# Kernel optimization log

Measured on AMD Instinct MI355X. Metric: run time of the kernel, lower is better.

The kernel has to match this reference:

```python
import jax, jax.numpy as jnp
import numpy as np

C = 64
NUM_HEADS = 8
HEAD_DIM = C // NUM_HEADS


def setup_inputs() -> dict:
    key = jax.random.key(0)
    ks = jax.random.split(key, 8)
    B, D, H, W = 1, 8, 24, 32
    s = 1.0 / np.sqrt(C)  # conv3d default init scale (approx)
    return {
        "x": jax.random.normal(ks[0], (B, C, D, H, W), dtype=jnp.float32),
        "wq": jax.random.normal(ks[1], (C, C), dtype=jnp.float32) * s,
        "bq": jax.random.normal(ks[2], (C,), dtype=jnp.float32) * s,
        "wk": jax.random.normal(ks[3], (C, C), dtype=jnp.float32) * s,
        "bk": jax.random.normal(ks[4], (C,), dtype=jnp.float32) * s,
        "wv": jax.random.normal(ks[5], (C, C), dtype=jnp.float32) * s,
        "bv": jax.random.normal(ks[6], (C,), dtype=jnp.float32) * s,
        "gamma": jnp.zeros((1,), dtype=jnp.float32),
    }


def _proj(x_flat, w, b):
    # x_flat: [B, C, N]; 1x1x1 conv == channel-mixing matmul
    return jnp.einsum("oc,bcn->bon", w, x_flat) + b[None, :, None]


def reference(x, wq, bq, wk, bk, wv, bv, gamma):
    B, Cc, D, Hh, W = x.shape
    N = D * Hh * W
    xf = x.reshape(B, Cc, N)
    # [B, heads, head_dim, N]
    q = _proj(xf, wq, bq).reshape(B, NUM_HEADS, HEAD_DIM, N)
    k = _proj(xf, wk, bk).reshape(B, NUM_HEADS, HEAD_DIM, N)
    v = _proj(xf, wv, bv).reshape(B, NUM_HEADS, HEAD_DIM, N)
    scale = 1.0 / np.sqrt(HEAD_DIM)
    # energy: [B, heads, N, N] = q^T k
    energy = jnp.einsum("bhdn,bhdm->bhnm", q, k) * scale
    attn = jax.nn.softmax(energy, axis=-1)
    # out: [B, heads, head_dim, N]
    out = jnp.einsum("bhnm,bhdm->bhdn", attn, v)
    out = out.reshape(B, Cc, D, Hh, W)
    return gamma * out + x
```

## Files before the change

### kernel.cpp

```cpp
#include <hip/hip_runtime.h>
#include <hip/hip_bf16.h>

typedef __attribute__((ext_vector_type(8)))  short  short8;
typedef __attribute__((ext_vector_type(16))) float  f32x16;

#define N_TOK 6144
#define NHEADS 8
#define TK 256
#define VPITCH (TK + 8)
#define QTILES 24

static __device__ __forceinline__ ushort f2bf(float f) {
    union { __hip_bfloat16 h; ushort u; } c;
    c.h = __float2bfloat16(f);
    return c.u;
}

static __device__ __forceinline__ uint packexp2(float s0, float s1) {
    float t0 = __builtin_fmaf(s0, 128.0f, 12599161.0f);
    float t1 = __builtin_fmaf(s1, 128.0f, 12599161.0f);
    return __builtin_amdgcn_perm(__float_as_uint(t1), __float_as_uint(t0), 0x05040100u);
}

__global__ __launch_bounds__(256)
void proj_kernel(const float* __restrict__ x,
                 const float* __restrict__ wq, const float* __restrict__ bq,
                 const float* __restrict__ wk, const float* __restrict__ bk,
                 const float* __restrict__ wv, const float* __restrict__ bv,
                 ushort* __restrict__ Qb, ushort* __restrict__ Kb, ushort* __restrict__ Vt)
{
    __shared__ float wql[512], wkl[512], wvl[512];
    const int b  = blockIdx.x;
    const int h  = b / 24;
    const int nt = b % 24;
    const int t  = threadIdx.x;

    for (int i = t; i < 512; i += 256) {
        int row = i >> 6, col = i & 63;
        wql[i] = wq[(h * 8 + row) * 64 + col];
        wkl[i] = wk[(h * 8 + row) * 64 + col];
        wvl[i] = wv[(h * 8 + row) * 64 + col];
    }
    __syncthreads();

    const int n = nt * 256 + t;
    float accq[8], acck[8], accv[8];
#pragma unroll
    for (int d = 0; d < 8; ++d) { accq[d] = 0.f; acck[d] = 0.f; accv[d] = 0.f; }

    for (int c = 0; c < 64; c += 4) {
        float x0 = x[(c + 0) * N_TOK + n];
        float x1 = x[(c + 1) * N_TOK + n];
        float x2 = x[(c + 2) * N_TOK + n];
        float x3 = x[(c + 3) * N_TOK + n];
#pragma unroll
        for (int d = 0; d < 8; ++d) {
            float4 wqv = *(const float4*)&wql[d * 64 + c];
            float4 wkv = *(const float4*)&wkl[d * 64 + c];
            float4 wvv = *(const float4*)&wvl[d * 64 + c];
            accq[d] += wqv.x * x0 + wqv.y * x1 + wqv.z * x2 + wqv.w * x3;
            acck[d] += wkv.x * x0 + wkv.y * x1 + wkv.z * x2 + wkv.w * x3;
            accv[d] += wvv.x * x0 + wvv.y * x1 + wvv.z * x2 + wvv.w * x3;
        }
    }

    const float qscale = 0.5100700982081662f;
    union { ushort us[8]; uint4 v; } qo, ko;
#pragma unroll
    for (int d = 0; d < 8; ++d) {
        qo.us[d] = f2bf((accq[d] + bq[h * 8 + d]) * qscale);
        ko.us[d] = f2bf(acck[d] + bk[h * 8 + d]);
    }
    size_t base = ((size_t)h * N_TOK + n) * 8;
    *(uint4*)&Qb[base] = qo.v;
    *(uint4*)&Kb[base] = ko.v;

    const int j  = n & 15;
    const int jp = ((j & 12) == 4) ? j + 4 : (((j & 12) == 8) ? j - 4 : j);
    const int np = (n & ~15) | jp;
#pragma unroll
    for (int d = 0; d < 8; ++d)
        Vt[((size_t)(h * 8 + d)) * N_TOK + np] = f2bf(accv[d] + bv[h * 8 + d]);
}

__global__ __launch_bounds__(256)
void attn_kernel(const ushort* __restrict__ Qb, const ushort* __restrict__ Kb,
                 const ushort* __restrict__ Vt,
                 float* __restrict__ partL, float* __restrict__ partO,
                 int KS, int NK)
{
    __shared__ __align__(16) ushort Klds[TK * 8];
    __shared__ __align__(16) ushort Vlds[9 * VPITCH];

    const int b     = blockIdx.x;
    const int slice = b / (NHEADS * QTILES);
    const int rem   = b - slice * (NHEADS * QTILES);
    const int h     = rem / QTILES;
    const int qt    = rem - h * QTILES;
    const int tid   = threadIdx.x;
    const int lane  = tid & 63;
    const int qi    = lane & 31;
    const int hi    = lane >> 5;
    const int q0    = qt * 256 + (tid >> 6) * 64 + qi;

    {
        uint* v8 = (uint*)&Vlds[8 * VPITCH];
        if (tid < 128) v8[tid] = 0x3F803F80u;
    }

    union { uint4 u; short8 s; } qf0, qf1;
    qf0.u = make_uint4(0u, 0u, 0u, 0u);
    qf1.u = make_uint4(0u, 0u, 0u, 0u);
    if (hi == 0) {
        qf0.u = *(const uint4*)&Qb[((size_t)h * N_TOK + q0) * 8];
        qf1.u = *(const uint4*)&Qb[((size_t)h * N_TOK + q0 + 32) * 8];
    }

    f32x16 o0, o1, zc;
#pragma unroll
    for (int i = 0; i < 16; ++i) { o0[i] = 0.f; o1[i] = 0.f; zc[i] = 0.f; }

    const ushort* kbase = &Klds[qi * 8];
    const int     vrow  = (qi < 8) ? qi : 8;
    const ushort* vbase = &Vlds[vrow * VPITCH + hi * 8];
    const int     k0g   = slice * NK;

    const uint4* kg = (const uint4*)&Kb[((size_t)h * N_TOK + k0g) * 8];
    const uint4* vg = (const uint4*)&Vt[((size_t)(h * 8 + (tid >> 5))) * N_TOK + k0g];
    const int    vchunk = tid & 31;
    uint4* kdst = &((uint4*)Klds)[tid];
    uint4* vdst = (uint4*)&Vlds[(tid >> 5) * VPITCH + vchunk * 8];

    uint4 ksA = kg[tid];
    uint4 vsA = vg[vchunk];

    const int nt = NK / TK;
    for (int tile = 0; tile < nt; ++tile) {
        __syncthreads();
        *kdst = ksA;
        *vdst = vsA;
        __syncthreads();

        if (tile + 1 < nt) {
            ksA = kg[(tile + 1) * TK + tid];
            vsA = vg[(tile + 1) * (TK / 8) + vchunk];
        }

#pragma unroll
        for (int ks = 0; ks < TK / 32; ++ks) {
            short8 kf = *(const short8*)(kbase + ks * 256);
            f32x16 s0 = __builtin_amdgcn_mfma_f32_32x32x16_bf16(kf, qf0.s, zc, 0, 0, 0);
            f32x16 s1 = __builtin_amdgcn_mfma_f32_32x32x16_bf16(kf, qf1.s, zc, 0, 0, 0);

            union { uint4 u; short8 s8; } a0, a1, b0, b1;
            a0.u = make_uint4(packexp2(s0[0],  s0[1]),  packexp2(s0[2],  s0[3]),
                              packexp2(s0[4],  s0[5]),  packexp2(s0[6],  s0[7]));
            b0.u = make_uint4(packexp2(s0[8],  s0[9]),  packexp2(s0[10], s0[11]),
                              packexp2(s0[12], s0[13]), packexp2(s0[14], s0[15]));
            a1.u = make_uint4(packexp2(s1[0],  s1[1]),  packexp2(s1[2],  s1[3]),
                              packexp2(s1[4],  s1[5]),  packexp2(s1[6],  s1[7]));
            b1.u = make_uint4(packexp2(s1[8],  s1[9]),  packexp2(s1[10], s1[11]),
                              packexp2(s1[12], s1[13]), packexp2(s1[14], s1[15]));

            short8 vf0 = *(const short8*)(vbase + ks * 32);
            short8 vf1 = *(const short8*)(vbase + ks * 32 + 16);
            o0 = __builtin_amdgcn_mfma_f32_32x32x16_bf16(vf0, a0.s8, o0, 0, 0, 0);
            o0 = __builtin_amdgcn_mfma_f32_32x32x16_bf16(vf1, b0.s8, o0, 0, 0, 0);
            o1 = __builtin_amdgcn_mfma_f32_32x32x16_bf16(vf0, a1.s8, o1, 0, 0, 0);
            o1 = __builtin_amdgcn_mfma_f32_32x32x16_bf16(vf1, b1.s8, o1, 0, 0, 0);
        }
    }

    const size_t pb0 = ((size_t)(h * KS + slice)) * N_TOK + q0;
    if (hi == 0) {
        partL[pb0]      = o0[4];
        partL[pb0 + 32] = o1[4];
    }
    *(float4*)&partO[pb0 * 8 + 4 * hi]        = make_float4(o0[0], o0[1], o0[2], o0[3]);
    *(float4*)&partO[(pb0 + 32) * 8 + 4 * hi] = make_float4(o1[0], o1[1], o1[2], o1[3]);
}

__global__ __launch_bounds__(256)
void combine_kernel(const float* __restrict__ partL, const float* __restrict__ partO,
                    const float* __restrict__ x, const float* __restrict__ gamma,
                    float* __restrict__ y, int KS)
{
    const int g = blockIdx.x * 256 + threadIdx.x;
    const int h = g / N_TOK;
    const int q = g - h * N_TOK;

    float L = 0.f;
    float o[8];
#pragma unroll
    for (int d = 0; d < 8; ++d) o[d] = 0.f;
    for (int s = 0; s < KS; ++s) {
        size_t pb = ((size_t)(h * KS + s)) * N_TOK + q;
        L += partL[pb];
        const float4* po = (const float4*)&partO[pb * 8];
        float4 a = po[0], bv = po[1];
        o[0] += a.x;  o[1] += a.y;  o[2] += a.z;  o[3] += a.w;
        o[4] += bv.x; o[5] += bv.y; o[6] += bv.z; o[7] += bv.w;
    }
    float inv = 1.0f / L;
    float gam = gamma[0];
#pragma unroll
    for (int d = 0; d < 8; ++d) {
        size_t idx = ((size_t)(h * 8 + d)) * N_TOK + q;
        y[idx] = gam * (o[d] * inv) + x[idx];
    }
}

extern "C" void kernel_launch(void* const* d_in, const int* in_sizes, int n_in,
                              void* d_out, int out_size, void* d_ws, size_t ws_size,
                              hipStream_t stream) {
    const float* x     = (const float*)d_in[0];
    const float* wq    = (const float*)d_in[1];
    const float* bq    = (const float*)d_in[2];
    const float* wk    = (const float*)d_in[3];
    const float* bk    = (const float*)d_in[4];
    const float* wv    = (const float*)d_in[5];
    const float* bv    = (const float*)d_in[6];
    const float* gamma = (const float*)d_in[7];
    float* y = (float*)d_out;

    char* wsb = (char*)d_ws;
    const size_t bfB = (size_t)NHEADS * N_TOK * 8 * 2;
    ushort* Qb = (ushort*)wsb;
    ushort* Kb = (ushort*)(wsb + bfB);
    ushort* Vt = (ushort*)(wsb + 2 * bfB);

    int KS = 8;
    while (KS > 1) {
        size_t need = 3 * bfB + (size_t)KS * ((size_t)NHEADS * N_TOK * 4
                                            + (size_t)NHEADS * N_TOK * 8 * 4);
        if (need <= ws_size) break;
        KS >>= 1;
    }
    const int NK = N_TOK / KS;

    float* partL = (float*)(wsb + 3 * bfB);
    float* partO = partL + (size_t)NHEADS * N_TOK * KS;

    proj_kernel<<<192, 256, 0, stream>>>(x, wq, bq, wk, bk, wv, bv, Qb, Kb, Vt);
    attn_kernel<<<KS * NHEADS * QTILES, 256, 0, stream>>>(Qb, Kb, Vt, partL, partO, KS, NK);
    combine_kernel<<<192, 256, 0, stream>>>(partL, partO, x, gamma, y, KS);
}
```

Baseline: 50.09 us.

## Fuse split-K combine into attention kernel via last-block atomic counter

Removes the separate combine kernel. Each attention block now bumps a per-(head, q-tile) atomic counter after writing its partial results, and the last slice to finish reduces all partials and writes the output. The projection kernel zeroes the counters. This saves one kernel launch and its dispatch gap, at the cost of thread fences, an atomic per block, and a serialized tail on whichever block finishes last.

```diff
diff --git a/kernel.cpp b/kernel.cpp
--- a/kernel.cpp
+++ b/kernel.cpp
@@ -27,13 +27,16 @@
                  const float* __restrict__ wq, const float* __restrict__ bq,
                  const float* __restrict__ wk, const float* __restrict__ bk,
                  const float* __restrict__ wv, const float* __restrict__ bv,
-                 ushort* __restrict__ Qb, ushort* __restrict__ Kb, ushort* __restrict__ Vt)
+                 ushort* __restrict__ Qb, ushort* __restrict__ Kb, ushort* __restrict__ Vt,
+                 int* __restrict__ cnt)
 {
     __shared__ float wql[512], wkl[512], wvl[512];
     const int b  = blockIdx.x;
     const int h  = b / 24;
     const int nt = b % 24;
     const int t  = threadIdx.x;
+
+    if (t == 0) cnt[b] = 0;
 
     for (int i = t; i < 512; i += 256) {
         int row = i >> 6, col = i & 63;
@@ -87,10 +90,13 @@
 void attn_kernel(const ushort* __restrict__ Qb, const ushort* __restrict__ Kb,
                  const ushort* __restrict__ Vt,
                  float* __restrict__ partL, float* __restrict__ partO,
+                 const float* __restrict__ x, const float* __restrict__ gamma,
+                 float* __restrict__ y, int* __restrict__ cnt,
                  int KS, int NK)
 {
     __shared__ __align__(16) ushort Klds[TK * 8];
     __shared__ __align__(16) ushort Vlds[9 * VPITCH];
+    __shared__ int lastFlag;
 
     const int b     = blockIdx.x;
     const int slice = b / (NHEADS * QTILES);
@@ -178,35 +184,35 @@
     }
     *(float4*)&partO[pb0 * 8 + 4 * hi]        = make_float4(o0[0], o0[1], o0[2], o0[3]);
     *(float4*)&partO[(pb0 + 32) * 8 + 4 * hi] = make_float4(o1[0], o1[1], o1[2], o1[3]);
-}
-
-__global__ __launch_bounds__(256)
-void combine_kernel(const float* __restrict__ partL, const float* __restrict__ partO,
-                    const float* __restrict__ x, const float* __restrict__ gamma,
-                    float* __restrict__ y, int KS)
-{
-    const int g = blockIdx.x * 256 + threadIdx.x;
-    const int h = g / N_TOK;
-    const int q = g - h * N_TOK;
-
+
+    __threadfence();
+    if (tid == 0) {
+        int old = __atomic_fetch_add(&cnt[h * QTILES + qt], 1, __ATOMIC_RELAXED);
+        lastFlag = (old == KS - 1);
+    }
+    __syncthreads();
+    if (!lastFlag) return;
+    __threadfence();
+
+    const int qq = qt * 256 + tid;
     float L = 0.f;
-    float o[8];
-#pragma unroll
-    for (int d = 0; d < 8; ++d) o[d] = 0.f;
-    for (int s = 0; s < KS; ++s) {
-        size_t pb = ((size_t)(h * KS + s)) * N_TOK + q;
+    float oc[8];
+#pragma unroll
+    for (int d = 0; d < 8; ++d) oc[d] = 0.f;
+    for (int s2 = 0; s2 < KS; ++s2) {
+        size_t pb = ((size_t)(h * KS + s2)) * N_TOK + qq;
         L += partL[pb];
         const float4* po = (const float4*)&partO[pb * 8];
         float4 a = po[0], bv = po[1];
-        o[0] += a.x;  o[1] += a.y;  o[2] += a.z;  o[3] += a.w;
-        o[4] += bv.x; o[5] += bv.y; o[6] += bv.z; o[7] += bv.w;
+        oc[0] += a.x;  oc[1] += a.y;  oc[2] += a.z;  oc[3] += a.w;
+        oc[4] += bv.x; oc[5] += bv.y; oc[6] += bv.z; oc[7] += bv.w;
     }
     float inv = 1.0f / L;
     float gam = gamma[0];
 #pragma unroll
     for (int d = 0; d < 8; ++d) {
-        size_t idx = ((size_t)(h * 8 + d)) * N_TOK + q;
-        y[idx] = gam * (o[d] * inv) + x[idx];
+        size_t idx = ((size_t)(h * 8 + d)) * N_TOK + qq;
+        y[idx] = gam * (oc[d] * inv) + x[idx];
     }
 }
 
@@ -232,7 +238,8 @@
     int KS = 8;
     while (KS > 1) {
         size_t need = 3 * bfB + (size_t)KS * ((size_t)NHEADS * N_TOK * 4
-                                            + (size_t)NHEADS * N_TOK * 8 * 4);
+                                            + (size_t)NHEADS * N_TOK * 8 * 4)
+                    + NHEADS * QTILES * sizeof(int);
         if (need <= ws_size) break;
         KS >>= 1;
     }
@@ -240,8 +247,9 @@
 
     float* partL = (float*)(wsb + 3 * bfB);
     float* partO = partL + (size_t)NHEADS * N_TOK * KS;
-
-    proj_kernel<<<192, 256, 0, stream>>>(x, wq, bq, wk, bk, wv, bv, Qb, Kb, Vt);
-    attn_kernel<<<KS * NHEADS * QTILES, 256, 0, stream>>>(Qb, Kb, Vt, partL, partO, KS, NK);
-    combine_kernel<<<192, 256, 0, stream>>>(partL, partO, x, gamma, y, KS);
-}
+    int*   cnt   = (int*)(partO + (size_t)NHEADS * N_TOK * KS * 8);
+
+    proj_kernel<<<192, 256, 0, stream>>>(x, wq, bq, wk, bk, wv, bv, Qb, Kb, Vt, cnt);
+    attn_kernel<<<KS * NHEADS * QTILES, 256, 0, stream>>>(Qb, Kb, Vt, partL, partO,
+                                                          x, gamma, y, cnt, KS, NK);
+}
```

New measurement: 186.8 us. +272.9%, slower.
